# Kernel optimization log

Measured on AMD Instinct MI355X. Metric: run time of the kernel, lower is better.

Reference implementation:

```python
import jax, jax.numpy as jnp
import numpy as np

# dims (see shape_source)
N = 100000          # num_ent
E = 400000          # num edges
B = 2048            # batch of (sub, rel) queries
INIT_DIM = 100
UFD = 100           # user_fe_dim
ENT_DIM = INIT_DIM + 3 * UFD   # feature_method='concat' -> 400
H = 2               # attention heads
D = 64              # per-head dim
GCN = H * D         # gcn_dim = embed_dim = 128 (gcn_layer == 1)
NUM_REL = 50
NR2 = 2 * NUM_REL


def setup_inputs() -> dict:
    key = jax.random.key(0)
    ks = jax.random.split(key, 17)
    inp = {}
    # constructor / forward int tensors
    inp["edge_index"] = jax.random.randint(ks[0], (2, E), 0, N, dtype=jnp.int32)
    inp["edge_type"] = jax.random.randint(ks[1], (E,), 0, NR2, dtype=jnp.int32)
    inp["edge_type_p"] = jax.random.randint(ks[2], (E,), 0, NR2, dtype=jnp.int32)
    inp["ent_feature"] = jax.random.randint(ks[3], (N, 3), 0, 3, dtype=jnp.int32)
    inp["sub"] = jax.random.randint(ks[4], (B,), 0, N, dtype=jnp.int32)
    inp["rel"] = jax.random.randint(ks[5], (B,), 0, NR2, dtype=jnp.int32)
    inp["relp"] = jax.random.randint(ks[6], (B,), 0, NR2, dtype=jnp.int32)
    # learned parameters
    s = 0.02
    inp["id_embed"] = jax.random.normal(ks[7], (N, INIT_DIM), jnp.float32) * s
    inp["gender_tab"] = jax.random.normal(ks[8], (3, UFD), jnp.float32) * s
    inp["age_tab"] = jax.random.normal(ks[9], (9, UFD), jnp.float32) * s
    inp["level_tab"] = jax.random.normal(ks[10], (11, UFD), jnp.float32) * s
    inp["init_rel"] = jax.random.normal(ks[11], (NR2, ENT_DIM), jnp.float32) * s
    inp["W"] = jax.random.normal(ks[12], (ENT_DIM, H * D), jnp.float32) * 0.05
    inp["Wr"] = jax.random.normal(ks[13], (ENT_DIM, H * D), jnp.float32) * 0.05
    inp["att_src"] = jax.random.normal(ks[14], (H, D), jnp.float32) * 0.05
    inp["att_dst"] = jax.random.normal(ks[15], (H, D), jnp.float32) * 0.05
    inp["Wrel"] = jax.random.normal(ks[16], (ENT_DIM, GCN), jnp.float32) * 0.05
    return inp


def _segment_softmax(logits, seg, num_segments):
    # logits: [E, H], seg: [E] destination node ids
    m = jax.ops.segment_max(logits, seg, num_segments=num_segments)
    ex = jnp.exp(logits - m[seg])
    den = jax.ops.segment_sum(ex, seg, num_segments=num_segments)
    return ex / (den[seg] + 1e-16)


def _rghat_conv(x, rel_emb, edge_index, edge_type, W, Wr, att_src, att_dst, Wrel):
    # relational multi-head graph attention (RGHATConv)
    n = x.shape[0]
    h = (x @ W).reshape(n, H, D)                       # [N,H,D] projected nodes
    r_proj = (rel_emb @ Wr).reshape(-1, H, D)          # [R,H,D]
    src, dst = edge_index[0], edge_index[1]
    msg = h[src] + r_proj[edge_type]                   # [E,H,D] edge messages
    logits = jax.nn.leaky_relu(
        jnp.sum(msg * att_src, axis=-1) + jnp.sum(h[dst] * att_dst, axis=-1),
        negative_slope=0.2,
    )                                                  # [E,H]
    alpha = _segment_softmax(logits, dst, n)           # per-destination softmax
    out = jax.ops.segment_sum(alpha[..., None] * msg, dst, num_segments=n)
    out = jnp.tanh(out.reshape(n, H * D))              # [N,GCN]
    r_out = rel_emb @ Wrel                             # [R,GCN]
    return out, r_out


def reference(edge_index, edge_type, edge_type_p, ent_feature, sub, rel, relp,
              id_embed, gender_tab, age_tab, level_tab, init_rel,
              W, Wr, att_src, att_dst, Wrel):
    # feature_method == 'concat': gather per-node feature embeddings and concat
    x1 = gender_tab[ent_feature[:, 0]]
    x2 = age_tab[ent_feature[:, 1]]
    x3 = level_tab[ent_feature[:, 2]]
    init_embed = jnp.concatenate([id_embed, x1, x2, x3], axis=1)  # [N, ENT_DIM]
    # single conv layer (gcn_layer == 1); dropouts are identity in eval
    x, r = _rghat_conv(init_embed, init_rel, edge_index, edge_type,
                       W, Wr, att_src, att_dst, Wrel)
    sub_emb = x[sub]                                   # index_select gather
    # add_parent_rel == False -> r returned whole (relp unused)
    return (sub_emb, r, x)
```

## Files before the change

kernel.cpp:

```cpp
#include <hip/hip_runtime.h>
#include <hip/hip_bf16.h>
#include <hip/hip_fp16.h>

#define N_NODES 100000
#define E_EDGES 400000
#define B_SUB 2048
#define INIT_DIM 100
#define UFD 100
#define ENT_DIM 400
#define GCN 128
#define NR2 100
#define KPAD 416
#define NCH 13
#define CHK 32
#define CAP 64

typedef __attribute__((ext_vector_type(8))) short shortx8;
typedef __attribute__((ext_vector_type(4))) float floatx4;

#define OUT_R_OFF ((long)B_SUB * GCN)
#define OUT_X_OFF ((long)(B_SUB + NR2) * GCN)

__device__ __forceinline__ unsigned short f2b(float f) {
    unsigned u = __float_as_uint(f);
    u += 0x7fffu + ((u >> 16) & 1u);
    return (unsigned short)(u >> 16);
}
__device__ __forceinline__ unsigned pk2(float x, float y) {
    return (unsigned)f2b(x) | ((unsigned)f2b(y) << 16);
}
__device__ __forceinline__ unsigned cvtpk2(float x, float y) {
    unsigned r;
    asm("v_cvt_pk_bf16_f32 %0, %1, %2" : "=v"(r) : "v"(x), "v"(y));
    return r;
}
__device__ __forceinline__ float blo(unsigned u) { return __uint_as_float(u << 16); }
__device__ __forceinline__ float bhi(unsigned u) { return __uint_as_float(u & 0xFFFF0000u); }

__device__ __forceinline__ float fast_tanh(float x) {
    float e2 = __expf(2.f * x);
    return 1.f - 2.f / (e2 + 1.f);
}

__global__ void wt_kernel(const float* __restrict__ W, unsigned short* __restrict__ Wt,
                          int* __restrict__ cursor) {
    int idx = blockIdx.x * 256 + threadIdx.x;
    if (idx < GCN * KPAD) {
        int n = idx & 127, k = idx >> 7;
        unsigned short o = 0;
        if (k < ENT_DIM) o = f2b(W[(long)k * GCN + n]);
        Wt[(long)n * KPAD + k] = o;
    }
    if (idx < N_NODES) cursor[idx] = 0;
}

__global__ __launch_bounds__(256) void rel_kernel(
        const float* __restrict__ init_rel, const float* __restrict__ Wr,
        const float* __restrict__ Wrel, const float* __restrict__ att_src,
        unsigned* __restrict__ rp_b, float* __restrict__ rproj_att,
        float* __restrict__ out_r) {
    int rel = blockIdx.x;
    int t = threadIdx.x;
    int tx = t & 127, kh = t >> 7;
    __shared__ float rl[ENT_DIM];
    __shared__ float p1[2][128], p2[2][128];
    __shared__ float accbuf[128];
    for (int k = t; k < ENT_DIM; k += 256) rl[k] = init_rel[(long)rel * ENT_DIM + k];
    __syncthreads();
    float a1 = 0.f, a2 = 0.f;
    {
        const float* wr = Wr + (long)(kh * 200) * GCN + tx;
        const float* wl = Wrel + (long)(kh * 200) * GCN + tx;
        const float* rv = rl + kh * 200;
#pragma unroll 8
        for (int k = 0; k < 200; ++k) {
            float v = rv[k];
            a1 += v * wr[(long)k * GCN];
            a2 += v * wl[(long)k * GCN];
        }
    }
    p1[kh][tx] = a1;
    p2[kh][tx] = a2;
    __syncthreads();
    if (t < 128) {
        float acc1 = p1[0][tx] + p1[1][tx];
        float acc2 = p2[0][tx] + p2[1][tx];
        out_r[rel * GCN + tx] = acc2;
        accbuf[tx] = acc1;
        int head = tx >> 6, d = tx & 63;
        float v = acc1 * att_src[head * 64 + d];
        for (int off = 32; off > 0; off >>= 1) v += __shfl_down(v, off, 64);
        if (d == 0) rproj_att[rel * 2 + head] = v;
    }
    __syncthreads();
    if (t < 64) rp_b[rel * 64 + t] = pk2(accbuf[t], accbuf[t + 64]);
}

__global__ __launch_bounds__(256) void hgemm_kernel(
        const float* __restrict__ id_embed, const float* __restrict__ gtab,
        const float* __restrict__ atab, const float* __restrict__ ltab,
        const int* __restrict__ ent_feature, const unsigned short* __restrict__ Wt,
        const float* __restrict__ att_src, const float* __restrict__ att_dst,
        unsigned* __restrict__ h_b, float* __restrict__ hsrc_att, float* __restrict__ hdst_att) {
    __shared__ __align__(16) float As[2][64 * CHK];
    __shared__ __align__(16) unsigned short Bs[2][128 * CHK];

    int t = threadIdx.x;
    int w = t >> 6, lane = t & 63, quad = lane >> 4, l16 = lane & 15;
    int n0 = blockIdx.x * 64;

    int rA = t >> 3;
    int lA4 = ((t & 7) ^ (rA & 7)) * 4;
    const float* segp[2][4];
#pragma unroll
    for (int rr = 0; rr < 2; ++rr) {
        int node = n0 + rr * 32 + rA;
        int nc = node < N_NODES ? node : N_NODES - 1;
        segp[rr][0] = id_embed + (long)nc * INIT_DIM;
        segp[rr][1] = gtab + ent_feature[nc * 3] * UFD;
        segp[rr][2] = atab + ent_feature[nc * 3 + 1] * UFD;
        segp[rr][3] = ltab + ent_feature[nc * 3 + 2] * UFD;
    }
    int cB = t >> 2;
    int lB8 = ((t & 3) ^ ((t >> 3) & 3)) * 8;
    const unsigned short* bsrc0 = Wt + (long)cB * KPAD + lB8;
    const unsigned short* bsrc1 = Wt + (long)(64 + cB) * KPAD + lB8;

#define SEGPTR(rr_, kg_) ((kg_) < 100 ? segp[rr_][0] + (kg_) : \
                          (kg_) < 200 ? segp[rr_][1] + ((kg_) - 100) : \
                          (kg_) < 300 ? segp[rr_][2] + ((kg_) - 200) : \
                          (kg_) < 400 ? segp[rr_][3] + ((kg_) - 300) : segp[rr_][0])

#define STAGE(ch_, bi_) { \
    int kgA_ = (ch_) * CHK + lA4; \
    __builtin_amdgcn_global_load_lds( \
        (const __attribute__((address_space(1))) unsigned*)SEGPTR(0, kgA_), \
        (__attribute__((address_space(3))) unsigned*)((char*)&As[bi_][0] + w * 1024), 16, 0, 0); \
    __builtin_amdgcn_global_load_lds( \
        (const __attribute__((address_space(1))) unsigned*)SEGPTR(1, kgA_), \
        (__attribute__((address_space(3))) unsigned*)((char*)&As[bi_][0] + 4096 + w * 1024), 16, 0, 0); \
    __builtin_amdgcn_global_load_lds( \
        (const __attribute__((address_space(1))) unsigned*)(bsrc0 + (ch_) * CHK), \
        (__attribute__((address_space(3))) unsigned*)((char*)&Bs[bi_][0] + w * 1024), 16, 0, 0); \
    __builtin_amdgcn_global_load_lds( \
        (const __attribute__((address_space(1))) unsigned*)(bsrc1 + (ch_) * CHK), \
        (__attribute__((address_space(3))) unsigned*)((char*)&Bs[bi_][0] + 4096 + w * 1024), 16, 0, 0); \
}

    floatx4 acc[8];
#pragma unroll
    for (int c = 0; c < 8; ++c) acc[c] = (floatx4){0.f, 0.f, 0.f, 0.f};

    int xA0 = (2 * quad) ^ (l16 & 7);
    int xA1 = (2 * quad + 1) ^ (l16 & 7);
    int qB = quad ^ ((l16 >> 1) & 3);

#define COMPUTE(bi_) { \
    const float* arow_ = &As[bi_][0] + (w * 16 + l16) * CHK; \
    float4 fa0_ = *(const float4*)(arow_ + xA0 * 4); \
    float4 fa1_ = *(const float4*)(arow_ + xA1 * 4); \
    uint4 u_; \
    u_.x = cvtpk2(fa0_.x, fa0_.y); u_.y = cvtpk2(fa0_.z, fa0_.w); \
    u_.z = cvtpk2(fa1_.x, fa1_.y); u_.w = cvtpk2(fa1_.z, fa1_.w); \
    shortx8 af_ = *(shortx8*)&u_; \
    _Pragma("unroll") for (int c = 0; c < 8; ++c) { \
        shortx8 b_ = *(const shortx8*)(&Bs[bi_][0] + (c * 16 + l16) * CHK + qB * 8); \
        acc[c] = __builtin_amdgcn_mfma_f32_16x16x32_bf16(af_, b_, acc[c], 0, 0, 0); \
    } \
}

    STAGE(0, 0);
#pragma unroll
    for (int ch = 0; ch < NCH; ++ch) {
        __syncthreads();
        if (ch + 1 < NCH) STAGE(ch + 1, (ch & 1) ^ 1);
        COMPUTE(ch & 1);
    }
#undef STAGE
#undef COMPUTE
#undef SEGPTR

    float attS_r[8], attD_r[8];
#pragma unroll
    for (int c = 0; c < 8; ++c) {
        attS_r[c] = att_src[c * 16 + l16];
        attD_r[c] = att_dst[c * 16 + l16];
    }
    int baseRow = n0 + w * 16 + quad * 4;
#pragma unroll
    for (int i = 0; i < 4; ++i) {
        int node = baseRow + i;
        bool ok = node < N_NODES;
#pragma unroll
        for (int c = 0; c < 4; ++c)
            if (ok) h_b[(long)node * 64 + c * 16 + l16] = cvtpk2(acc[c][i], acc[c + 4][i]);
        float s0 = 0.f, s1 = 0.f, d0 = 0.f, d1 = 0.f;
#pragma unroll
        for (int c = 0; c < 8; ++c) {
            float v = acc[c][i];
            if (c < 4) { s0 += v * attS_r[c]; d0 += v * attD_r[c]; }
            else       { s1 += v * attS_r[c]; d1 += v * attD_r[c]; }
        }
#pragma unroll
        for (int m = 1; m < 16; m <<= 1) {
            s0 += __shfl_xor(s0, m, 64);
            s1 += __shfl_xor(s1, m, 64);
            d0 += __shfl_xor(d0, m, 64);
            d1 += __shfl_xor(d1, m, 64);
        }
        if (ok && l16 == 0) {
            *(float2*)&hsrc_att[node * 2] = make_float2(s0, s1);
            *(float2*)&hdst_att[node * 2] = make_float2(d0, d1);
        }
    }
}

__global__ void fill_kernel(const int* __restrict__ edge_index, const int* __restrict__ edge_type,
                            int* __restrict__ cursor,
                            const float2* __restrict__ hsrc2, const float2* __restrict__ rpa2,
                            const float2* __restrict__ hdst2,
                            uint2* __restrict__ ebuf) {
    int e = blockIdx.x * blockDim.x + threadIdx.x;
    if (e >= E_EDGES) return;
    int src = edge_index[e];
    int dst = edge_index[E_EDGES + e];
    int et = edge_type[e];
    float2 hs = hsrc2[src];
    float2 ra = rpa2[et];
    float2 hd = hdst2[dst];
    float x0 = hs.x + ra.x + hd.x;
    float x1 = hs.y + ra.y + hd.y;
    x0 = x0 > 0.f ? x0 : 0.2f * x0;
    x1 = x1 > 0.f ? x1 : 0.2f * x1;
    __half2 hh = __floats2half2_rn(__expf(x0), __expf(x1));
    union { __half2 h; unsigned u; } cv; cv.h = hh;
    int pos = atomicAdd(&cursor[dst], 1);
    if (pos < CAP)
        ebuf[(long)dst * CAP + pos] = make_uint2(((unsigned)et << 17) | (unsigned)src, cv.u);
}

__global__ __launch_bounds__(256) void agg_kernel(
        const int* __restrict__ cursor, const uint2* __restrict__ ebuf,
        const unsigned* __restrict__ h_b, const unsigned* __restrict__ rp_b,
        float* __restrict__ out_x) {
    int w = threadIdx.x >> 6, l = threadIdx.x & 63;
    int dstA = (blockIdx.x * 4 + w) * 2;
    int dstB = dstA + 1;
    const uint4* baseA = (const uint4*)(ebuf + (long)dstA * CAP);
    const uint4* baseB = (const uint4*)(ebuf + (long)dstB * CAP);
    uint4 qA = baseA[0];
    uint4 qB = baseB[0];
    int cntA = cursor[dstA]; if (cntA > CAP) cntA = CAP;
    int cntB = cursor[dstB]; if (cntB > CAP) cntB = CAP;
    int jm = cntA > cntB ? cntA : cntB;

    float aA0 = 0.f, aA1 = 0.f, dA0 = 0.f, dA1 = 0.f;
    float aB0 = 0.f, aB1 = 0.f, dB0 = 0.f, dB1 = 0.f;

    for (int j = 0; j < jm; j += 2) {
        unsigned iA0 = j     < cntA ? qA.x : 0u, eA0u = j     < cntA ? qA.y : 0u;
        unsigned iA1 = j + 1 < cntA ? qA.z : 0u, eA1u = j + 1 < cntA ? qA.w : 0u;
        unsigned iB0 = j     < cntB ? qB.x : 0u, eB0u = j     < cntB ? qB.y : 0u;
        unsigned iB1 = j + 1 < cntB ? qB.z : 0u, eB1u = j + 1 < cntB ? qB.w : 0u;
        if (j + 2 < jm) {
            qA = baseA[(j >> 1) + 1];
            qB = baseB[(j >> 1) + 1];
        }
        unsigned hbA0 = h_b[(long)(iA0 & 0x1FFFF) * 64 + l];
        unsigned hbA1 = h_b[(long)(iA1 & 0x1FFFF) * 64 + l];
        unsigned hbB0 = h_b[(long)(iB0 & 0x1FFFF) * 64 + l];
        unsigned hbB1 = h_b[(long)(iB1 & 0x1FFFF) * 64 + l];
        unsigned rbA0 = rp_b[(iA0 >> 17) * 64 + l];
        unsigned rbA1 = rp_b[(iA1 >> 17) * 64 + l];
        unsigned rbB0 = rp_b[(iB0 >> 17) * 64 + l];
        unsigned rbB1 = rp_b[(iB1 >> 17) * 64 + l];
        union { __half2 h; unsigned u; } cA0, cA1, cB0, cB1;
        cA0.u = eA0u; cA1.u = eA1u; cB0.u = eB0u; cB1.u = eB1u;
        float2 fA0 = __half22float2(cA0.h), fA1 = __half22float2(cA1.h);
        float2 fB0 = __half22float2(cB0.h), fB1 = __half22float2(cB1.h);
        aA0 += fA0.x * (blo(hbA0) + blo(rbA0)) + fA1.x * (blo(hbA1) + blo(rbA1));
        aA1 += fA0.y * (bhi(hbA0) + bhi(rbA0)) + fA1.y * (bhi(hbA1) + bhi(rbA1));
        aB0 += fB0.x * (blo(hbB0) + blo(rbB0)) + fB1.x * (blo(hbB1) + blo(rbB1));
        aB1 += fB0.y * (bhi(hbB0) + bhi(rbB0)) + fB1.y * (bhi(hbB1) + bhi(rbB1));
        dA0 += fA0.x + fA1.x;  dA1 += fA0.y + fA1.y;
        dB0 += fB0.x + fB1.x;  dB1 += fB0.y + fB1.y;
    }
    float rA0 = __builtin_amdgcn_rcpf(dA0 + 1e-16f);
    float rA1 = __builtin_amdgcn_rcpf(dA1 + 1e-16f);
    float rB0 = __builtin_amdgcn_rcpf(dB0 + 1e-16f);
    float rB1 = __builtin_amdgcn_rcpf(dB1 + 1e-16f);
    __builtin_nontemporal_store(fast_tanh(aA0 * rA0), &out_x[(long)dstA * GCN + l]);
    __builtin_nontemporal_store(fast_tanh(aA1 * rA1), &out_x[(long)dstA * GCN + 64 + l]);
    __builtin_nontemporal_store(fast_tanh(aB0 * rB0), &out_x[(long)dstB * GCN + l]);
    __builtin_nontemporal_store(fast_tanh(aB1 * rB1), &out_x[(long)dstB * GCN + 64 + l]);
}

__global__ void gather_kernel(const int* __restrict__ sub, const float* __restrict__ out_x,
                              float* __restrict__ out_sub) {
    int idx = blockIdx.x * blockDim.x + threadIdx.x;
    if (idx >= B_SUB * GCN) return;
    int b = idx >> 7, d = idx & 127;
    out_sub[idx] = out_x[(long)sub[b] * GCN + d];
}

extern "C" void kernel_launch(void* const* d_in, const int* in_sizes, int n_in,
                              void* d_out, int out_size, void* d_ws, size_t ws_size,
                              hipStream_t stream) {
    const int* edge_index = (const int*)d_in[0];
    const int* edge_type  = (const int*)d_in[1];
    const int* ent_feature = (const int*)d_in[3];
    const int* sub = (const int*)d_in[4];
    const float* id_embed = (const float*)d_in[7];
    const float* gtab = (const float*)d_in[8];
    const float* atab = (const float*)d_in[9];
    const float* ltab = (const float*)d_in[10];
    const float* init_rel = (const float*)d_in[11];
    const float* W = (const float*)d_in[12];
    const float* Wr = (const float*)d_in[13];
    const float* att_src = (const float*)d_in[14];
    const float* att_dst = (const float*)d_in[15];
    const float* Wrel = (const float*)d_in[16];

    char* ws = (char*)d_ws;
    unsigned* h_b = (unsigned*)ws;                          ws += (long)N_NODES * 64 * 4;
    unsigned* rp_b = (unsigned*)ws;                         ws += (long)NR2 * 64 * 4;
    float* rproj_att = (float*)ws;                          ws += NR2 * 2 * 4;
    float* hsrc_att = (float*)ws;                           ws += (long)N_NODES * 2 * 4;
    float* hdst_att = (float*)ws;                           ws += (long)N_NODES * 2 * 4;
    unsigned short* Wt = (unsigned short*)ws;               ws += (long)GCN * KPAD * 2;
    int* cursor = (int*)ws;                                 ws += (long)N_NODES * 4;
    uint2* ebuf = (uint2*)ws;                               ws += (long)N_NODES * CAP * 8;

    float* out = (float*)d_out;
    float* out_sub = out;
    float* out_r = out + OUT_R_OFF;
    float* out_x = out + OUT_X_OFF;

    const int NB = (N_NODES + 255) / 256;

    wt_kernel<<<NB, 256, 0, stream>>>(W, Wt, cursor);
    rel_kernel<<<NR2, 256, 0, stream>>>(init_rel, Wr, Wrel, att_src, rp_b, rproj_att, out_r);
    hgemm_kernel<<<(N_NODES + 63) / 64, 256, 0, stream>>>(id_embed, gtab, atab, ltab,
                                                          ent_feature, Wt, att_src, att_dst,
                                                          h_b, hsrc_att, hdst_att);
    fill_kernel<<<(E_EDGES + 255) / 256, 256, 0, stream>>>(edge_index, edge_type, cursor,
                                                           (const float2*)hsrc_att,
                                                           (const float2*)rproj_att,
                                                           (const float2*)hdst_att, ebuf);
    agg_kernel<<<N_NODES / 8, 256, 0, stream>>>(cursor, ebuf, h_b, rp_b, out_x);
    gather_kernel<<<(B_SUB * GCN + 255) / 256, 256, 0, stream>>>(sub, out_x, out_sub);
}
```

Measured before the change: 229.7 us.

## Load GEMM A-operand directly into registers instead of staging through LDS

The hgemm kernel stops staging the fp32 feature rows (A operand) in shared memory. Each lane now loads its row's 8 floats straight from global memory into registers, prefetching one chunk ahead, and converts them to bf16 for the MFMA. LDS then holds only the weight tile, and launch bounds request 6 blocks per SM. This cuts LDS traffic and footprint to raise occupancy, but the global loads become less coalesced and their latency is hidden only by a one-chunk register prefetch.

```diff
diff --git a/kernel.cpp b/kernel.cpp
--- a/kernel.cpp
+++ b/kernel.cpp
@@ -96,49 +96,36 @@
     if (t < 64) rp_b[rel * 64 + t] = pk2(accbuf[t], accbuf[t + 64]);
 }
 
-__global__ __launch_bounds__(256) void hgemm_kernel(
+__global__ __launch_bounds__(256, 6) void hgemm_kernel(
         const float* __restrict__ id_embed, const float* __restrict__ gtab,
         const float* __restrict__ atab, const float* __restrict__ ltab,
         const int* __restrict__ ent_feature, const unsigned short* __restrict__ Wt,
         const float* __restrict__ att_src, const float* __restrict__ att_dst,
         unsigned* __restrict__ h_b, float* __restrict__ hsrc_att, float* __restrict__ hdst_att) {
-    __shared__ __align__(16) float As[2][64 * CHK];
     __shared__ __align__(16) unsigned short Bs[2][128 * CHK];
 
     int t = threadIdx.x;
     int w = t >> 6, lane = t & 63, quad = lane >> 4, l16 = lane & 15;
     int n0 = blockIdx.x * 64;
 
-    int rA = t >> 3;
-    int lA4 = ((t & 7) ^ (rA & 7)) * 4;
-    const float* segp[2][4];
-#pragma unroll
-    for (int rr = 0; rr < 2; ++rr) {
-        int node = n0 + rr * 32 + rA;
-        int nc = node < N_NODES ? node : N_NODES - 1;
-        segp[rr][0] = id_embed + (long)nc * INIT_DIM;
-        segp[rr][1] = gtab + ent_feature[nc * 3] * UFD;
-        segp[rr][2] = atab + ent_feature[nc * 3 + 1] * UFD;
-        segp[rr][3] = ltab + ent_feature[nc * 3 + 2] * UFD;
-    }
+    int nrow = n0 + w * 16 + l16;
+    int nc = nrow < N_NODES ? nrow : N_NODES - 1;
+    const float* pid = id_embed + (long)nc * INIT_DIM;
+    const float* pg  = gtab + ent_feature[nc * 3] * UFD;
+    const float* pa  = atab + ent_feature[nc * 3 + 1] * UFD;
+    const float* pl  = ltab + ent_feature[nc * 3 + 2] * UFD;
+
     int cB = t >> 2;
     int lB8 = ((t & 3) ^ ((t >> 3) & 3)) * 8;
     const unsigned short* bsrc0 = Wt + (long)cB * KPAD + lB8;
     const unsigned short* bsrc1 = Wt + (long)(64 + cB) * KPAD + lB8;
 
-#define SEGPTR(rr_, kg_) ((kg_) < 100 ? segp[rr_][0] + (kg_) : \
-                          (kg_) < 200 ? segp[rr_][1] + ((kg_) - 100) : \
-                          (kg_) < 300 ? segp[rr_][2] + ((kg_) - 200) : \
-                          (kg_) < 400 ? segp[rr_][3] + ((kg_) - 300) : segp[rr_][0])
+#define SEGPTR(kg_) ((kg_) < 100 ? pid + (kg_) : \
+                     (kg_) < 200 ? pg + ((kg_) - 100) : \
+                     (kg_) < 300 ? pa + ((kg_) - 200) : \
+                     (kg_) < 400 ? pl + ((kg_) - 300) : pid)
 
 #define STAGE(ch_, bi_) { \
-    int kgA_ = (ch_) * CHK + lA4; \
-    __builtin_amdgcn_global_load_lds( \
-        (const __attribute__((address_space(1))) unsigned*)SEGPTR(0, kgA_), \
-        (__attribute__((address_space(3))) unsigned*)((char*)&As[bi_][0] + w * 1024), 16, 0, 0); \
-    __builtin_amdgcn_global_load_lds( \
-        (const __attribute__((address_space(1))) unsigned*)SEGPTR(1, kgA_), \
-        (__attribute__((address_space(3))) unsigned*)((char*)&As[bi_][0] + 4096 + w * 1024), 16, 0, 0); \
     __builtin_amdgcn_global_load_lds( \
         (const __attribute__((address_space(1))) unsigned*)(bsrc0 + (ch_) * CHK), \
         (__attribute__((address_space(3))) unsigned*)((char*)&Bs[bi_][0] + w * 1024), 16, 0, 0); \
@@ -151,33 +138,32 @@
 #pragma unroll
     for (int c = 0; c < 8; ++c) acc[c] = (floatx4){0.f, 0.f, 0.f, 0.f};
 
-    int xA0 = (2 * quad) ^ (l16 & 7);
-    int xA1 = (2 * quad + 1) ^ (l16 & 7);
     int qB = quad ^ ((l16 >> 1) & 3);
 
-#define COMPUTE(bi_) { \
-    const float* arow_ = &As[bi_][0] + (w * 16 + l16) * CHK; \
-    float4 fa0_ = *(const float4*)(arow_ + xA0 * 4); \
-    float4 fa1_ = *(const float4*)(arow_ + xA1 * 4); \
-    uint4 u_; \
-    u_.x = cvtpk2(fa0_.x, fa0_.y); u_.y = cvtpk2(fa0_.z, fa0_.w); \
-    u_.z = cvtpk2(fa1_.x, fa1_.y); u_.w = cvtpk2(fa1_.z, fa1_.w); \
-    shortx8 af_ = *(shortx8*)&u_; \
-    _Pragma("unroll") for (int c = 0; c < 8; ++c) { \
-        shortx8 b_ = *(const shortx8*)(&Bs[bi_][0] + (c * 16 + l16) * CHK + qB * 8); \
-        acc[c] = __builtin_amdgcn_mfma_f32_16x16x32_bf16(af_, b_, acc[c], 0, 0, 0); \
-    } \
-}
-
     STAGE(0, 0);
+    float4 va = *(const float4*)SEGPTR(quad * 8);
+    float4 vb = *(const float4*)SEGPTR(quad * 8 + 4);
+
 #pragma unroll
     for (int ch = 0; ch < NCH; ++ch) {
         __syncthreads();
         if (ch + 1 < NCH) STAGE(ch + 1, (ch & 1) ^ 1);
-        COMPUTE(ch & 1);
+        uint4 u_;
+        u_.x = cvtpk2(va.x, va.y); u_.y = cvtpk2(va.z, va.w);
+        u_.z = cvtpk2(vb.x, vb.y); u_.w = cvtpk2(vb.z, vb.w);
+        shortx8 af_ = *(shortx8*)&u_;
+        if (ch + 1 < NCH) {
+            int kg = (ch + 1) * CHK + quad * 8;
+            va = *(const float4*)SEGPTR(kg);
+            vb = *(const float4*)SEGPTR(kg + 4);
+        }
+#pragma unroll
+        for (int c = 0; c < 8; ++c) {
+            shortx8 b_ = *(const shortx8*)(&Bs[ch & 1][0] + (c * 16 + l16) * CHK + qB * 8);
+            acc[c] = __builtin_amdgcn_mfma_f32_16x16x32_bf16(af_, b_, acc[c], 0, 0, 0);
+        }
     }
 #undef STAGE
-#undef COMPUTE
 #undef SEGPTR
 
     float attS_r[8], attD_r[8];
```

Measured after the change: 228.8 us. Within noise of the previous version (-0.4%).
